# Performance work log

Measured on AMD Instinct MI355X. Metric: run time of the kernel, lower is better.

The kernel has to match this reference:

```python
import jax, jax.numpy as jnp
import numpy as np

B, H, IN, OUT = 8192, 1024, 4, 4


def setup_inputs() -> dict:
    key = jax.random.key(0)
    ks = jax.random.split(key, 16)
    s = 1.0 / np.sqrt(H)

    def p(k, shape):
        return jax.random.uniform(k, shape, jnp.float32, -s, s)

    return {
        "context": jax.random.normal(ks[0], (B, H), jnp.float32),
        "wc": p(ks[1], (H // 2, H)),
        "bc": p(ks[2], (H // 2,)),
        "gru1_wi": p(ks[3], (3 * H, H // 2)),
        "gru1_wh": p(ks[4], (3 * H, H)),
        "gru1_bi": p(ks[5], (3 * H,)),
        "gru1_bh": p(ks[6], (3 * H,)),
        "gru2_wi": p(ks[7], (3 * H, H // 2)),
        "gru2_wh": p(ks[8], (3 * H, H)),
        "gru2_bi": p(ks[9], (3 * H,)),
        "gru2_bh": p(ks[10], (3 * H,)),
        "fc_in_w": p(ks[11], (IN, H)),
        "fc_in_b": p(ks[12], (IN,)),
        "fc_out_w": p(ks[13], (OUT, H)),
        "fc_out_b": p(ks[14], (OUT,)),
        "future_length": 30,
        "past_length": 60,
    }


def _gru_unroll(ec, h0, wi, wh, bi, bh, length):
    """Run a PyTorch-semantics GRUCell `length` steps with constant input ec.

    Returns all hidden states stacked: [T, B, H].
    """
    # Input-side gates are constant across steps (input is always ec).
    gi = ec @ wi.T + bi                     # [B, 3H]
    i_r, i_z, i_n = jnp.split(gi, 3, axis=-1)

    def step(h, _):
        gh = h @ wh.T + bh                  # [B, 3H]
        h_r, h_z, h_n = jnp.split(gh, 3, axis=-1)
        r = jax.nn.sigmoid(i_r + h_r)
        z = jax.nn.sigmoid(i_z + h_z)
        n = jnp.tanh(i_n + r * h_n)
        h_new = (1.0 - z) * n + z * h
        return h_new, h_new

    _, hs = jax.lax.scan(step, h0, None, length=length)
    return hs  # [T, B, H]


def reference(context, wc, bc,
              gru1_wi, gru1_wh, gru1_bi, gru1_bh,
              gru2_wi, gru2_wh, gru2_bi, gru2_bh,
              fc_in_w, fc_in_b, fc_out_w, fc_out_b,
              future_length, past_length):
    # encoded_context = relu(context_encoder(context))
    ec = jax.nn.relu(context @ wc.T + bc)   # [B, H/2]

    # Training-mode past-reconstruction branch (decoder1 + fc_in).
    hs1 = _gru_unroll(ec, context, gru1_wi, gru1_wh, gru1_bi, gru1_bh, past_length)
    decoded_inputs = jnp.einsum('tbh,ih->bti', hs1, fc_in_w) + fc_in_b  # [B, T_past, IN]

    # Future-prediction branch (decoder2 + relu + fc_out).
    hs2 = _gru_unroll(ec, context, gru2_wi, gru2_wh, gru2_bi, gru2_bh, future_length)
    outputs = jnp.einsum('tbh,oh->bto', jax.nn.relu(hs2), fc_out_w) + fc_out_b  # [B, T_fut, OUT]

    return (decoded_inputs, outputs)
```

## Files before the change

### kernel.cpp

```cpp
#include <hip/hip_runtime.h>
#include <math.h>

typedef __bf16 bf16;
typedef __bf16 bf16x8 __attribute__((ext_vector_type(8)));
typedef float f32x4 __attribute__((ext_vector_type(4)));

#define B_DIM 8192
#define H_DIM 1024
#define T_PAST 60
#define T_FUT 30

static __device__ __forceinline__ void gld_lds16(const void* g, void* l) {
  __builtin_amdgcn_global_load_lds(
      (const __attribute__((address_space(1))) void*)g,
      (__attribute__((address_space(3))) void*)l, 16, 0, 0);
}

static __device__ __forceinline__ float sigm(float x) {
  return 1.f / (1.f + __expf(-x));
}
static __device__ __forceinline__ float tanh_fast(float x) {
  float xc = fminf(fmaxf(x, -10.f), 10.f);
  float e = __expf(2.f * xc);
  return (e - 1.f) / (e + 1.f);
}

__global__ void detect_dtype(const unsigned int* __restrict__ words,
                             int* __restrict__ is_bf16) {
  const int lane = threadIdx.x;
  int cnt = 0;
  for (int i = 0; i < 64; i++) {
    const unsigned int w = words[lane + i * 64];
    const int e = (w >> 7) & 0xFF;
    cnt += (e >= 100 && e <= 135) ? 1 : 0;
  }
  for (int off = 32; off > 0; off >>= 1) cnt += __shfl_down(cnt, off);
  if (lane == 0) *is_bf16 = (cnt >= 2048) ? 1 : 0;
}

struct ConvDesc { const void* src; bf16* dst; int n; };
struct ConvPack { ConvDesc d[15]; };

__global__ __launch_bounds__(256) void convert_all(ConvPack p,
                                                   const int* __restrict__ flag,
                                                   float* __restrict__ h0a,
                                                   float* __restrict__ h0b) {
  const int ti = blockIdx.y;
  const ConvDesc d = p.d[ti];
  const int bf = *flag;
  const long stride = (long)gridDim.x * 256 * 8;
  for (long base = ((long)blockIdx.x * 256 + threadIdx.x) * 8; base < d.n;
       base += stride) {
    if (base + 8 <= d.n) {
      float f[8];
      if (bf) {
        const uint4 v = *(const uint4*)((const char*)d.src + base * 2);
        *(uint4*)((char*)d.dst + base * 2) = v;
        if (ti == 0 && h0a) {
          const bf16* bv = (const bf16*)&v;
#pragma unroll
          for (int e = 0; e < 8; e++) f[e] = (float)bv[e];
        }
      } else {
        const float* s = (const float*)d.src + base;
        const float4 v0 = *(const float4*)s;
        const float4 v1 = *(const float4*)(s + 4);
        f[0] = v0.x; f[1] = v0.y; f[2] = v0.z; f[3] = v0.w;
        f[4] = v1.x; f[5] = v1.y; f[6] = v1.z; f[7] = v1.w;
        bf16 o[8];
#pragma unroll
        for (int e = 0; e < 8; e++) o[e] = (bf16)f[e];
        *(uint4*)((char*)d.dst + base * 2) = *(const uint4*)o;
      }
      if (ti == 0 && h0a) {
#pragma unroll
        for (int e = 0; e < 8; e++) { h0a[base + e] = f[e]; h0b[base + e] = f[e]; }
      }
    } else {
      for (long e = base; e < d.n; e++) {
        const float f = bf ? (float)((const bf16*)d.src)[e]
                           : ((const float*)d.src)[e];
        d.dst[e] = (bf16)f;
        if (ti == 0 && h0a) { h0a[e] = f; h0b[e] = f; }
      }
    }
  }
}

template <bool RELU, bool GI_BIAS>
__global__ __launch_bounds__(256, 2) void gemm_bt(
    const bf16* __restrict__ A, const bf16* __restrict__ Bm,
    const bf16* __restrict__ bias1, const bf16* __restrict__ bias2,
    bf16* __restrict__ C, int K, int N)
{
  __shared__ __attribute__((aligned(16))) bf16 As[128 * 32];
  __shared__ __attribute__((aligned(16))) bf16 Bs[128 * 32];
  const int tid = threadIdx.x;
  const int wave = tid >> 6, lane = tid & 63;
  const int quad = lane >> 4, l16 = lane & 15;
  const int m0 = blockIdx.x * 128, n0 = blockIdx.y * 128;
  const int wm = (wave & 1) * 64, wn = (wave >> 1) * 64;
  f32x4 acc[4][4] = {};
  for (int k0 = 0; k0 < K; k0 += 32) {
#pragma unroll
    for (int rr = 0; rr < 2; rr++) {
      const int c = rr * 256 + tid;
      const int cg = (c & 3) ^ ((c >> 3) & 3);
      gld_lds16(A + (size_t)(m0 + (c >> 2)) * K + (k0 + cg * 8),
                As + (size_t)(rr * 256 + wave * 64) * 8);
      gld_lds16(Bm + (size_t)(n0 + (c >> 2)) * K + (k0 + cg * 8),
                Bs + (size_t)(rr * 256 + wave * 64) * 8);
    }
    __syncthreads();
    bf16x8 af[4], bv[4];
#pragma unroll
    for (int t = 0; t < 4; t++) {
      const int ra = wm + t * 16 + l16;
      const int rb = wn + t * 16 + l16;
      af[t] = *(const bf16x8*)(As + (ra * 32 + (quad ^ ((ra >> 1) & 3)) * 8));
      bv[t] = *(const bf16x8*)(Bs + (rb * 32 + (quad ^ ((rb >> 1) & 3)) * 8));
    }
#pragma unroll
    for (int tm = 0; tm < 4; tm++)
#pragma unroll
      for (int tn = 0; tn < 4; tn++)
        acc[tm][tn] = __builtin_amdgcn_mfma_f32_16x16x32_bf16(af[tm], bv[tn], acc[tm][tn], 0, 0, 0);
    __syncthreads();
  }
#pragma unroll
  for (int tn = 0; tn < 4; tn++) {
    const int col = n0 + wn + tn * 16 + l16;
    float bias = (float)bias1[col];
    if (GI_BIAS) {
      if (col < 2 * H_DIM) bias += (float)bias2[col];
    }
#pragma unroll
    for (int tm = 0; tm < 4; tm++) {
#pragma unroll
      for (int r = 0; r < 4; r++) {
        const int row = m0 + wm + tm * 16 + quad * 4 + r;
        float v = acc[tm][tn][r] + bias;
        if (RELU) v = fmaxf(v, 0.f);
        C[(size_t)row * N + col] = (bf16)v;
      }
    }
  }
}

struct GruArgs {
  const bf16* h_in16; const float* h_in32;
  bf16* h_out16; float* h_out32;
  const bf16* gi;
  const bf16* wh;
  const bf16* bh;
  const bf16* fcw;
  float* proj;
  int projT, t, relu;
};

__global__ __launch_bounds__(256, 3) void gru_step(GruArgs g1, GruArgs g2)
{
  const GruArgs G = (blockIdx.z == 0) ? g1 : g2;
  __shared__ __attribute__((aligned(16))) bf16 As[64 * 32];
  __shared__ __attribute__((aligned(16))) bf16 Bs[192 * 32];
  const int tid = threadIdx.x;
  const int wave = tid >> 6, lane = tid & 63;
  const int quad = lane >> 4, l16 = lane & 15;
  const int m0 = blockIdx.x * 64;
  const int j0 = blockIdx.y * 64;
  f32x4 acc[12] = {};
  for (int k0 = 0; k0 < H_DIM; k0 += 32) {
    {
      const int c = tid;
      const int cg = (c & 3) ^ ((c >> 3) & 3);
      gld_lds16(G.h_in16 + (size_t)(m0 + (c >> 2)) * H_DIM + (k0 + cg * 8),
                As + (size_t)(wave * 64) * 8);
    }
#pragma unroll
    for (int rr = 0; rr < 3; rr++) {
      const int c = rr * 256 + tid;
      const int p = c >> 2;
      const int cg = (c & 3) ^ ((c >> 3) & 3);
      const int grow = (p >> 6) * H_DIM + j0 + (p & 63);
      gld_lds16(G.wh + (size_t)grow * H_DIM + (k0 + cg * 8),
                Bs + (size_t)(rr * 256 + wave * 64) * 8);
    }
    __syncthreads();
    const int ra = wave * 16 + l16;
    bf16x8 af = *(const bf16x8*)(As + (ra * 32 + (quad ^ ((ra >> 1) & 3)) * 8));
#pragma unroll
    for (int tn = 0; tn < 12; tn++) {
      const int rb = tn * 16 + l16;
      bf16x8 bv = *(const bf16x8*)(Bs + (rb * 32 + (quad ^ ((rb >> 1) & 3)) * 8));
      acc[tn] = __builtin_amdgcn_mfma_f32_16x16x32_bf16(af, bv, acc[tn], 0, 0, 0);
    }
    __syncthreads();
  }
  float pp[4][4];
#pragma unroll
  for (int r = 0; r < 4; r++)
#pragma unroll
    for (int i = 0; i < 4; i++) pp[r][i] = 0.f;

#pragma unroll
  for (int tj = 0; tj < 4; tj++) {
    const int j = j0 + tj * 16 + l16;
    const float bhn = (float)G.bh[2 * H_DIM + j];
    float fw[4];
#pragma unroll
    for (int i = 0; i < 4; i++) fw[i] = (float)G.fcw[i * H_DIM + j];
#pragma unroll
    for (int r = 0; r < 4; r++) {
      const int row = m0 + wave * 16 + quad * 4 + r;
      const size_t gb = (size_t)row * (3 * H_DIM) + j;
      const float gr = (float)G.gi[gb];
      const float gz = (float)G.gi[gb + H_DIM];
      const float gn = (float)G.gi[gb + 2 * H_DIM];
      const float hr = acc[tj][r];
      const float hz = acc[tj + 4][r];
      const float hn = acc[tj + 8][r];
      const float rg = sigm(gr + hr);
      const float zg = sigm(gz + hz);
      const float ng = tanh_fast(gn + rg * (hn + bhn));
      const size_t hidx = (size_t)row * H_DIM + j;
      const float hold = G.h_in32 ? G.h_in32[hidx] : (float)G.h_in16[hidx];
      const float hnew = (1.f - zg) * ng + zg * hold;
      if (G.h_out32) G.h_out32[hidx] = hnew;
      G.h_out16[hidx] = (bf16)hnew;
      const float act = G.relu ? fmaxf(hnew, 0.f) : hnew;
#pragma unroll
      for (int i = 0; i < 4; i++) pp[r][i] += fw[i] * act;
    }
  }
#pragma unroll
  for (int r = 0; r < 4; r++)
#pragma unroll
    for (int i = 0; i < 4; i++) {
      float v = pp[r][i];
      v += __shfl_xor(v, 1);
      v += __shfl_xor(v, 2);
      v += __shfl_xor(v, 4);
      v += __shfl_xor(v, 8);
      if (l16 == 0) {
        const int row = m0 + wave * 16 + quad * 4 + r;
        atomicAdd(&G.proj[((size_t)row * G.projT + G.t) * 4 + i], v);
      }
    }
}

__global__ __launch_bounds__(256) void finalize(const float* __restrict__ p1,
                                                const float* __restrict__ p2,
                                                const bf16* __restrict__ fib,
                                                const bf16* __restrict__ fob,
                                                const int* __restrict__ flag,
                                                void* __restrict__ out, int n) {
  const int idx = blockIdx.x * 256 + threadIdx.x;
  if (idx >= n) return;
  const int R1 = B_DIM * T_PAST * 4;
  float v;
  if (idx < R1) {
    v = p1[idx] + (float)fib[idx & 3];
  } else {
    const int k = idx - R1;
    v = p2[k] + (float)fob[k & 3];
  }
  if (*flag) ((bf16*)out)[idx] = (bf16)v;
  else       ((float*)out)[idx] = v;
}

extern "C" void kernel_launch(void* const* d_in, const int* in_sizes, int n_in,
                              void* d_out, int out_size, void* d_ws, size_t ws_size,
                              hipStream_t stream)
{
  (void)n_in;
  char* w = (char*)d_ws;
  auto alloc = [&](size_t bytes) -> void* {
    void* p = (void*)w;
    w += (bytes + 255) & ~(size_t)255;
    return p;
  };
  int* flag = (int*)alloc(256);

  bf16* canon[15];
  for (int i = 0; i < 15; i++) canon[i] = (bf16*)alloc((size_t)in_sizes[i] * 2);
  const bf16* ctx  = canon[0];
  const bf16* wc   = canon[1];
  const bf16* bc   = canon[2];
  const bf16* g1wi = canon[3];
  const bf16* g1wh = canon[4];
  const bf16* g1bi = canon[5];
  const bf16* g1bh = canon[6];
  const bf16* g2wi = canon[7];
  const bf16* g2wh = canon[8];
  const bf16* g2bi = canon[9];
  const bf16* g2bh = canon[10];
  const bf16* fiw  = canon[11];
  const bf16* fib  = canon[12];
  const bf16* fow  = canon[13];
  const bf16* fob  = canon[14];

  bf16* ec   = (bf16*)alloc((size_t)B_DIM * 512 * 2);
  bf16* gi1  = (bf16*)alloc((size_t)B_DIM * 3 * H_DIM * 2);
  bf16* gi2  = (bf16*)alloc((size_t)B_DIM * 3 * H_DIM * 2);
  bf16* h116[2] = {(bf16*)alloc((size_t)B_DIM * H_DIM * 2), (bf16*)alloc((size_t)B_DIM * H_DIM * 2)};
  bf16* h216[2] = {(bf16*)alloc((size_t)B_DIM * H_DIM * 2), (bf16*)alloc((size_t)B_DIM * H_DIM * 2)};
  float* proj1 = (float*)alloc((size_t)B_DIM * T_PAST * 4 * 4);
  float* proj2 = (float*)alloc((size_t)B_DIM * T_FUT * 4 * 4);
  float* h132[2] = {nullptr, nullptr};
  float* h232[2] = {nullptr, nullptr};
  const size_t used = (size_t)(w - (char*)d_ws);
  const size_t fp32_need = (size_t)4 * B_DIM * H_DIM * 4 + 4096;
  const bool fp32h = (ws_size > used) && ((ws_size - used) >= fp32_need);
  if (fp32h) {
    h132[0] = (float*)alloc((size_t)B_DIM * H_DIM * 4);
    h132[1] = (float*)alloc((size_t)B_DIM * H_DIM * 4);
    h232[0] = (float*)alloc((size_t)B_DIM * H_DIM * 4);
    h232[1] = (float*)alloc((size_t)B_DIM * H_DIM * 4);
  }

  detect_dtype<<<1, 64, 0, stream>>>((const unsigned int*)d_in[0], flag);

  hipMemsetAsync(proj1, 0,
                 ((size_t)B_DIM * T_PAST * 4 + (size_t)B_DIM * T_FUT * 4) * 4, stream);

  ConvPack cp;
  for (int i = 0; i < 15; i++) { cp.d[i].src = d_in[i]; cp.d[i].dst = canon[i]; cp.d[i].n = in_sizes[i]; }
  convert_all<<<dim3(4096, 15), 256, 0, stream>>>(cp, flag,
      fp32h ? h132[0] : nullptr, fp32h ? h232[0] : nullptr);

  gemm_bt<true, false><<<dim3(64, 4), 256, 0, stream>>>(ctx, wc, bc, nullptr, ec, H_DIM, 512);
  gemm_bt<false, true><<<dim3(64, 24), 256, 0, stream>>>(ec, g1wi, g1bi, g1bh, gi1, 512, 3 * H_DIM);
  gemm_bt<false, true><<<dim3(64, 24), 256, 0, stream>>>(ec, g2wi, g2bi, g2bh, gi2, 512, 3 * H_DIM);

  for (int t = 0; t < T_PAST; t++) {
    const int si = t & 1, so = (t + 1) & 1;
    GruArgs a1;
    a1.h_in16 = (t == 0) ? ctx : h116[si];
    a1.h_in32 = fp32h ? h132[si] : nullptr;
    a1.h_out16 = h116[so];
    a1.h_out32 = fp32h ? h132[so] : nullptr;
    a1.gi = gi1; a1.wh = g1wh; a1.bh = g1bh; a1.fcw = fiw;
    a1.proj = proj1; a1.projT = T_PAST; a1.t = t; a1.relu = 0;
    if (t < T_FUT) {
      GruArgs a2;
      a2.h_in16 = (t == 0) ? ctx : h216[si];
      a2.h_in32 = fp32h ? h232[si] : nullptr;
      a2.h_out16 = h216[so];
      a2.h_out32 = fp32h ? h232[so] : nullptr;
      a2.gi = gi2; a2.wh = g2wh; a2.bh = g2bh; a2.fcw = fow;
      a2.proj = proj2; a2.projT = T_FUT; a2.t = t; a2.relu = 1;
      gru_step<<<dim3(128, 16, 2), 256, 0, stream>>>(a1, a2);
    } else {
      gru_step<<<dim3(128, 16, 1), 256, 0, stream>>>(a1, a1);
    }
  }

  finalize<<<dim3((out_size + 255) / 256), 256, 0, stream>>>(
      proj1, proj2, fib, fob, flag, d_out, out_size);
}
```

Baseline: 9.435 ms.

## Enlarge GRU step tile to 128 rows and use 32x32x16 MFMA

The recurrent GEMM tile grows from 64 to 128 batch rows per block, and each wave now computes a 64x32 sub-tile with 32x32x16 bf16 MFMAs instead of 16x16x32. This raises arithmetic intensity per LDS load and halves the number of blocks, which cuts redundant weight loads. The epilogue is remapped to the 32x32 accumulator layout, with a wider shuffle reduction for the fc projection. Occupancy drops from 3 to 2 blocks per CU, and register pressure rises.

```diff
diff --git a/kernel.cpp b/kernel.cpp
--- a/kernel.cpp
+++ b/kernel.cpp
@@ -4,6 +4,7 @@
 typedef __bf16 bf16;
 typedef __bf16 bf16x8 __attribute__((ext_vector_type(8)));
 typedef float f32x4 __attribute__((ext_vector_type(4)));
+typedef float f32x16 __attribute__((ext_vector_type(16)));
 
 #define B_DIM 8192
 #define H_DIM 1024
@@ -158,94 +159,117 @@
   int projT, t, relu;
 };
 
-__global__ __launch_bounds__(256, 3) void gru_step(GruArgs g1, GruArgs g2)
+__global__ __launch_bounds__(256, 2) void gru_step(GruArgs g1, GruArgs g2)
 {
   const GruArgs G = (blockIdx.z == 0) ? g1 : g2;
-  __shared__ __attribute__((aligned(16))) bf16 As[64 * 32];
+  __shared__ __attribute__((aligned(16))) bf16 As[128 * 32];
   __shared__ __attribute__((aligned(16))) bf16 Bs[192 * 32];
   const int tid = threadIdx.x;
   const int wave = tid >> 6, lane = tid & 63;
-  const int quad = lane >> 4, l16 = lane & 15;
-  const int m0 = blockIdx.x * 64;
+  const int half = lane >> 5, l32 = lane & 31;
+  const int m0 = blockIdx.x * 128;
   const int j0 = blockIdx.y * 64;
-  f32x4 acc[12] = {};
-  for (int k0 = 0; k0 < H_DIM; k0 += 32) {
-    {
-      const int c = tid;
+  const int Rw = (wave & 1) * 64;
+  const int jw = (wave >> 1) * 32;
+
+  f32x16 acc[2][3] = {};
+  for (int kt = 0; kt < 32; kt++) {
+    const int k0 = kt * 32;
+#pragma unroll
+    for (int i = 0; i < 2; i++) {
+      const int c = i * 256 + tid;
       const int cg = (c & 3) ^ ((c >> 3) & 3);
       gld_lds16(G.h_in16 + (size_t)(m0 + (c >> 2)) * H_DIM + (k0 + cg * 8),
-                As + (size_t)(wave * 64) * 8);
-    }
-#pragma unroll
-    for (int rr = 0; rr < 3; rr++) {
-      const int c = rr * 256 + tid;
+                As + (size_t)(i * 256 + wave * 64) * 8);
+    }
+#pragma unroll
+    for (int i = 0; i < 3; i++) {
+      const int c = i * 256 + tid;
       const int p = c >> 2;
       const int cg = (c & 3) ^ ((c >> 3) & 3);
       const int grow = (p >> 6) * H_DIM + j0 + (p & 63);
       gld_lds16(G.wh + (size_t)grow * H_DIM + (k0 + cg * 8),
-                Bs + (size_t)(rr * 256 + wave * 64) * 8);
+                Bs + (size_t)(i * 256 + wave * 64) * 8);
     }
     __syncthreads();
-    const int ra = wave * 16 + l16;
-    bf16x8 af = *(const bf16x8*)(As + (ra * 32 + (quad ^ ((ra >> 1) & 3)) * 8));
-#pragma unroll
-    for (int tn = 0; tn < 12; tn++) {
-      const int rb = tn * 16 + l16;
-      bf16x8 bv = *(const bf16x8*)(Bs + (rb * 32 + (quad ^ ((rb >> 1) & 3)) * 8));
-      acc[tn] = __builtin_amdgcn_mfma_f32_16x16x32_bf16(af, bv, acc[tn], 0, 0, 0);
-    }
+    bf16x8 af[2][2], bfr[3][2];
+#pragma unroll
+    for (int mi = 0; mi < 2; mi++)
+#pragma unroll
+      for (int st = 0; st < 2; st++) {
+        const int r = Rw + mi * 32 + l32;
+        const int cc = (st * 2 + half) ^ ((r >> 1) & 3);
+        af[mi][st] = *(const bf16x8*)(As + ((size_t)r * 4 + cc) * 8);
+      }
+#pragma unroll
+    for (int g = 0; g < 3; g++)
+#pragma unroll
+      for (int st = 0; st < 2; st++) {
+        const int p = g * 64 + jw + l32;
+        const int cc = (st * 2 + half) ^ ((p >> 1) & 3);
+        bfr[g][st] = *(const bf16x8*)(Bs + ((size_t)p * 4 + cc) * 8);
+      }
+#pragma unroll
+    for (int g = 0; g < 3; g++)
+#pragma unroll
+      for (int mi = 0; mi < 2; mi++) {
+        acc[mi][g] = __builtin_amdgcn_mfma_f32_32x32x16_bf16(af[mi][0], bfr[g][0], acc[mi][g], 0, 0, 0);
+        acc[mi][g] = __builtin_amdgcn_mfma_f32_32x32x16_bf16(af[mi][1], bfr[g][1], acc[mi][g], 0, 0, 0);
+      }
     __syncthreads();
   }
-  float pp[4][4];
-#pragma unroll
-  for (int r = 0; r < 4; r++)
-#pragma unroll
-    for (int i = 0; i < 4; i++) pp[r][i] = 0.f;
-
-#pragma unroll
-  for (int tj = 0; tj < 4; tj++) {
-    const int j = j0 + tj * 16 + l16;
-    const float bhn = (float)G.bh[2 * H_DIM + j];
-    float fw[4];
-#pragma unroll
-    for (int i = 0; i < 4; i++) fw[i] = (float)G.fcw[i * H_DIM + j];
-#pragma unroll
-    for (int r = 0; r < 4; r++) {
-      const int row = m0 + wave * 16 + quad * 4 + r;
-      const size_t gb = (size_t)row * (3 * H_DIM) + j;
-      const float gr = (float)G.gi[gb];
-      const float gz = (float)G.gi[gb + H_DIM];
-      const float gn = (float)G.gi[gb + 2 * H_DIM];
-      const float hr = acc[tj][r];
-      const float hz = acc[tj + 4][r];
-      const float hn = acc[tj + 8][r];
-      const float rg = sigm(gr + hr);
-      const float zg = sigm(gz + hz);
-      const float ng = tanh_fast(gn + rg * (hn + bhn));
-      const size_t hidx = (size_t)row * H_DIM + j;
-      const float hold = G.h_in32 ? G.h_in32[hidx] : (float)G.h_in16[hidx];
-      const float hnew = (1.f - zg) * ng + zg * hold;
-      if (G.h_out32) G.h_out32[hidx] = hnew;
-      G.h_out16[hidx] = (bf16)hnew;
-      const float act = G.relu ? fmaxf(hnew, 0.f) : hnew;
-#pragma unroll
-      for (int i = 0; i < 4; i++) pp[r][i] += fw[i] * act;
-    }
-  }
-#pragma unroll
-  for (int r = 0; r < 4; r++)
-#pragma unroll
-    for (int i = 0; i < 4; i++) {
-      float v = pp[r][i];
-      v += __shfl_xor(v, 1);
-      v += __shfl_xor(v, 2);
-      v += __shfl_xor(v, 4);
-      v += __shfl_xor(v, 8);
-      if (l16 == 0) {
-        const int row = m0 + wave * 16 + quad * 4 + r;
-        atomicAdd(&G.proj[((size_t)row * G.projT + G.t) * 4 + i], v);
-      }
-    }
+
+  const int jglob = j0 + jw + l32;
+  const float bhn = (float)G.bh[2 * H_DIM + jglob];
+  float fw[4];
+#pragma unroll
+  for (int i = 0; i < 4; i++) fw[i] = (float)G.fcw[i * H_DIM + jglob];
+
+#pragma unroll
+  for (int mi = 0; mi < 2; mi++) {
+#pragma unroll
+    for (int Q = 0; Q < 4; Q++) {
+      float pp[4][4];
+#pragma unroll
+      for (int r = 0; r < 4; r++) {
+        const int reg = Q * 4 + r;
+        const int row = m0 + Rw + mi * 32 + r + 8 * Q + 4 * half;
+        const size_t gb = (size_t)row * (3 * H_DIM) + jglob;
+        const float gr = (float)G.gi[gb];
+        const float gz = (float)G.gi[gb + H_DIM];
+        const float gn = (float)G.gi[gb + 2 * H_DIM];
+        const float hr = acc[mi][0][reg];
+        const float hz = acc[mi][1][reg];
+        const float hn = acc[mi][2][reg];
+        const float rg = sigm(gr + hr);
+        const float zg = sigm(gz + hz);
+        const float ng = tanh_fast(gn + rg * (hn + bhn));
+        const size_t hidx = (size_t)row * H_DIM + jglob;
+        const float hold = G.h_in32 ? G.h_in32[hidx] : (float)G.h_in16[hidx];
+        const float hnew = (1.f - zg) * ng + zg * hold;
+        if (G.h_out32) G.h_out32[hidx] = hnew;
+        G.h_out16[hidx] = (bf16)hnew;
+        const float act = G.relu ? fmaxf(hnew, 0.f) : hnew;
+#pragma unroll
+        for (int i = 0; i < 4; i++) pp[r][i] = fw[i] * act;
+      }
+#pragma unroll
+      for (int r = 0; r < 4; r++)
+#pragma unroll
+        for (int i = 0; i < 4; i++) {
+          float v = pp[r][i];
+          v += __shfl_xor(v, 1);
+          v += __shfl_xor(v, 2);
+          v += __shfl_xor(v, 4);
+          v += __shfl_xor(v, 8);
+          v += __shfl_xor(v, 16);
+          if (l32 == 0) {
+            const int row = m0 + Rw + mi * 32 + r + 8 * Q + 4 * half;
+            atomicAdd(&G.proj[((size_t)row * G.projT + G.t) * 4 + i], v);
+          }
+        }
+    }
+  }
 }
 
 __global__ __launch_bounds__(256) void finalize(const float* __restrict__ p1,
@@ -349,9 +373,9 @@
       a2.h_out32 = fp32h ? h232[so] : nullptr;
       a2.gi = gi2; a2.wh = g2wh; a2.bh = g2bh; a2.fcw = fow;
       a2.proj = proj2; a2.projT = T_FUT; a2.t = t; a2.relu = 1;
-      gru_step<<<dim3(128, 16, 2), 256, 0, stream>>>(a1, a2);
+      gru_step<<<dim3(64, 16, 2), 256, 0, stream>>>(a1, a2);
     } else {
-      gru_step<<<dim3(128, 16, 1), 256, 0, stream>>>(a1, a1);
+      gru_step<<<dim3(64, 16, 1), 256, 0, stream>>>(a1, a1);
     }
   }
 
```

Result: slower. 12.90 ms (+36.7%).
